# Optimization experiments

Measured on AMD Instinct MI355X. Metric: run time of the kernel, lower is better.

## Reference

```python
import jax, jax.numpy as jnp
import numpy as np

HEAD_NUM = 16

def setup_inputs() -> dict:
    key = jax.random.key(0)
    ks = jax.random.split(key, 5)
    B, N, D = 2, 2048, 1024
    x = jax.random.normal(ks[0], (B, N, D), dtype=jnp.float32)
    scale = 0.02
    W_q = jax.random.normal(ks[1], (D, D), dtype=jnp.float32) * scale
    W_k = jax.random.normal(ks[2], (D, D), dtype=jnp.float32) * scale
    W_v = jax.random.normal(ks[3], (D, D), dtype=jnp.float32) * scale
    W_o = jax.random.normal(ks[4], (D, D), dtype=jnp.float32) * scale
    return {"x": x, "W_q": W_q, "W_k": W_k, "W_v": W_v, "W_o": W_o}

def reference(x, W_q, W_k, W_v, W_o):
    B, N, D = x.shape
    H = HEAD_NUM
    hd = D // H  # head_dim
    inv_sqrt_hd = 1.0 / np.sqrt(hd).astype(np.float32)

    def split_head(t):
        # einops 'b n (d h) -> b h n d' : head index is the INNER factor
        return t.reshape(B, N, hd, H).transpose(0, 3, 1, 2)  # [B,H,N,hd]

    # nn.Linear(bias=False): y = x @ W.T
    Q = split_head(x @ W_q.T)
    K = split_head(x @ W_k.T)
    V = split_head(x @ W_v.T)

    scores = jnp.einsum('bhnd,bhmd->bhnm', Q, K) * inv_sqrt_hd  # [B,H,N,N]
    attn = jax.nn.softmax(scores, axis=-1)
    heads = jnp.einsum('bhnm,bhmd->bhnd', attn, V)  # [B,H,N,hd]

    # einops 'b h n d -> b n (h d)' : head index is the OUTER factor here
    concat = heads.transpose(0, 2, 1, 3).reshape(B, N, D)
    return concat @ W_o.T
```

## Files before the change

### kernel.cpp

```cpp
#include <hip/hip_runtime.h>
#include <hip/hip_bf16.h>

typedef __bf16 bf16_t;
typedef __attribute__((ext_vector_type(8))) __bf16 bf16x8;
typedef __attribute__((ext_vector_type(4))) __bf16 bf16x4;
typedef __attribute__((ext_vector_type(4))) float f32x4;
typedef __attribute__((ext_vector_type(16))) float f32x16;

#define MFMA16(A,B,C) __builtin_amdgcn_mfma_f32_16x16x32_bf16((A),(B),(C),0,0,0)
#define MFMA32(A,B,C) __builtin_amdgcn_mfma_f32_32x32x16_bf16((A),(B),(C),0,0,0)

#define BATCH 2
#define SEQ 2048
#define DMODEL 1024
#define NHEAD 16
#define HDIM 64
#define MROWS (BATCH * SEQ)

__device__ __forceinline__ void async16(const bf16_t* g, bf16_t* l) {
    __builtin_amdgcn_global_load_lds(
        (const __attribute__((address_space(1))) unsigned int*)g,
        (__attribute__((address_space(3))) unsigned int*)l, 16, 0, 0);
}

__device__ __forceinline__ bf16x8 ldsA32(const bf16_t* base, int row, int chunk) {
    return *(const bf16x8*)&base[row * 32 + ((chunk ^ ((row >> 1) & 3)) << 3)];
}
__device__ __forceinline__ bf16x8 ldsA64(const bf16_t* base, int row, int chunk) {
    return *(const bf16x8*)&base[row * 64 + ((chunk ^ (row & 7)) << 3)];
}

__device__ __forceinline__ unsigned pk(float a, float b) {
    union { unsigned u; bf16_t h[2]; } t;
    t.h[0] = (bf16_t)a;
    t.h[1] = (bf16_t)b;
    return t.u;
}

__global__ void split_kernel(const float* __restrict__ x, const float* __restrict__ Wq,
                             const float* __restrict__ Wk, const float* __restrict__ Wv,
                             const float* __restrict__ Wo, bf16_t* __restrict__ xh,
                             bf16_t* __restrict__ wh) {
    int blk = blockIdx.x;
    if (blk < 4096) {
        int i = blk * 256 + threadIdx.x;
        f32x4 v = ((const f32x4*)x)[i];
        bf16x4 h;
#pragma unroll
        for (int c = 0; c < 4; ++c) h[c] = (bf16_t)v[c];
        ((bf16x4*)xh)[i] = h;
        return;
    }
    int e = blk - 4096;
    int z = e >> 10;
    int i = (e & 1023) * 256 + threadIdx.x;
    const float* src = (z == 0) ? Wq : (z == 1) ? Wk : (z == 2) ? Wv : Wo;
    const float scale = (z == 0) ? 0.125f * 1.44269504088896f : 1.0f;
    int row = i >> 8, col4 = i & 255;
    int r_src;
    if (z < 3) {
        int h = row >> 6, d = row & 63;
        r_src = 16 * d + h;
    } else {
        r_src = row;
    }
    f32x4 v = ((const f32x4*)src)[r_src * 256 + col4];
    bf16x4 h4;
#pragma unroll
    for (int c = 0; c < 4; ++c) h4[c] = (bf16_t)(v[c] * scale);
    ((bf16x4*)(wh + (size_t)z * DMODEL * DMODEL))[i] = h4;
}

__global__ __launch_bounds__(256)
void gemm_qkv_kernel(const bf16_t* __restrict__ Ah, const bf16_t* __restrict__ Bh0,
                     bf16_t* __restrict__ Coh0, int M, int Nn, int Kk) {
    __shared__ __align__(16) bf16_t smem[2][8192];

    const int z = blockIdx.z;
    const bf16_t* Bh = Bh0 + (size_t)z * Nn * Kk;
    const int m0 = blockIdx.y * 128, n0 = blockIdx.x * 128;
    const int tid = threadIdx.x;
    const int wave = tid >> 6, lane = tid & 63, lq = lane >> 4, ln = lane & 15;
    const int wr = wave >> 1, wc = wave & 1;

    const bf16_t* g_ptr[4];
    int l_off[4];
#pragma unroll
    for (int q = 0; q < 4; ++q) {
        int e = wave * 4 + q;
        int a = e >> 3, u = e & 7;
        int C = u * 64 + lane;
        int r = C >> 2, p = C & 3;
        int c = p ^ ((r >> 1) & 3);
        g_ptr[q] = (a == 0 ? Ah + (size_t)(m0 + r) * Kk
                           : Bh + (size_t)(n0 + r) * Kk) + c * 8;
        l_off[q] = a * 4096 + u * 512;
    }

    f32x4 acc[4][4] = {};

#pragma unroll
    for (int q = 0; q < 4; ++q)
        async16(g_ptr[q], &smem[0][l_off[q]]);

    const int NIT = Kk / 32;
    for (int j = 0; j < NIT; ++j) {
        __syncthreads();
        if (j + 1 < NIT) {
#pragma unroll
            for (int q = 0; q < 4; ++q)
                async16(g_ptr[q] + (j + 1) * 32, &smem[(j + 1) & 1][l_off[q]]);
        }
        const bf16_t* cur = smem[j & 1];

        bf16x8 ah[4], bh[4];
#pragma unroll
        for (int t = 0; t < 4; ++t) {
            ah[t] = ldsA32(cur, wr * 64 + t * 16 + ln, lq);
            bh[t] = ldsA32(cur + 4096, wc * 64 + t * 16 + ln, lq);
        }
#pragma unroll
        for (int tm = 0; tm < 4; ++tm)
#pragma unroll
            for (int tn = 0; tn < 4; ++tn)
                acc[tm][tn] = MFMA16(ah[tm], bh[tn], acc[tm][tn]);
    }

#pragma unroll
    for (int tm = 0; tm < 4; ++tm)
#pragma unroll
        for (int tn = 0; tn < 4; ++tn)
#pragma unroll
            for (int p = 0; p < 4; ++p) {
                int gm = m0 + wr * 64 + tm * 16 + lq * 4 + p;
                int gn = n0 + wc * 64 + tn * 16 + ln;
                Coh0[(size_t)z * M * Nn + (size_t)gm * Nn + gn] =
                    (bf16_t)acc[tm][tn][p];
            }
}

__global__ __launch_bounds__(256)
void gemm_out_kernel(const bf16_t* __restrict__ Ah, const bf16_t* __restrict__ Bh,
                     float* __restrict__ Cf, int M, int Nn, int Kk) {
    __shared__ __align__(16) bf16_t smem[2][6144];

    const int m0 = blockIdx.y * 64, n0 = blockIdx.x * 128;
    const int tid = threadIdx.x;
    const int wave = tid >> 6, lane = tid & 63, lq = lane >> 4, ln = lane & 15;
    const int wr = wave >> 1, wc = wave & 1;

    const bf16_t* g_ptr[3];
    int l_off[3];
#pragma unroll
    for (int q = 0; q < 3; ++q) {
        int e = wave * 3 + q;
        const bf16_t* arr;
        int u, rowbase, lb;
        if (e < 4) { arr = Ah; u = e;     rowbase = m0; lb = 0; }
        else       { arr = Bh; u = e - 4; rowbase = n0; lb = 2048; }
        int r = u * 16 + (lane >> 2), p = lane & 3;
        int c = p ^ ((r >> 1) & 3);
        g_ptr[q] = arr + (size_t)(rowbase + r) * Kk + c * 8;
        l_off[q] = lb + u * 512;
    }

    f32x4 acc[2][4] = {};

#pragma unroll
    for (int q = 0; q < 3; ++q)
        async16(g_ptr[q], &smem[0][l_off[q]]);

    const int NIT = Kk / 32;
    for (int j = 0; j < NIT; ++j) {
        __syncthreads();
        if (j + 1 < NIT) {
#pragma unroll
            for (int q = 0; q < 3; ++q)
                async16(g_ptr[q] + (j + 1) * 32, &smem[(j + 1) & 1][l_off[q]]);
        }
        const bf16_t* cur = smem[j & 1];

        bf16x8 ah[2], bh[4];
#pragma unroll
        for (int t = 0; t < 2; ++t)
            ah[t] = ldsA32(cur, wr * 32 + t * 16 + ln, lq);
#pragma unroll
        for (int t = 0; t < 4; ++t)
            bh[t] = ldsA32(cur + 2048, wc * 64 + t * 16 + ln, lq);
#pragma unroll
        for (int tm = 0; tm < 2; ++tm)
#pragma unroll
            for (int tn = 0; tn < 4; ++tn)
                acc[tm][tn] = MFMA16(ah[tm], bh[tn], acc[tm][tn]);
    }

#pragma unroll
    for (int tm = 0; tm < 2; ++tm)
#pragma unroll
        for (int tn = 0; tn < 4; ++tn)
#pragma unroll
            for (int p = 0; p < 4; ++p) {
                int gm = m0 + wr * 32 + tm * 16 + lq * 4 + p;
                int gn = n0 + wc * 64 + tn * 16 + ln;
                Cf[(size_t)gm * Nn + gn] = acc[tm][tn][p];
            }
}

__global__ __launch_bounds__(256)
void vtrans_kernel(const bf16_t* __restrict__ Vn, bf16_t* __restrict__ Vt) {
    __shared__ bf16_t t[64][66];
    const int bh = blockIdx.y;
    const int b = bh >> 4, h = bh & 15;
    const int n0 = blockIdx.x * 64;
    const int tid = threadIdx.x;
#pragma unroll
    for (int it = 0; it < 2; ++it) {
        int c = it * 256 + tid;
        int r = c >> 3, p = c & 7;
        *(bf16x8*)&t[r][p * 8] =
            *(const bf16x8*)&Vn[((size_t)(b * SEQ + n0 + r)) * DMODEL + h * HDIM + p * 8];
    }
    __syncthreads();
#pragma unroll
    for (int it = 0; it < 2; ++it) {
        int c = it * 256 + tid;
        int d = c >> 3, p = c & 7;
        bf16x8 v;
#pragma unroll
        for (int e = 0; e < 8; ++e) v[e] = t[p * 8 + e][d];
        *(bf16x8*)&Vt[((size_t)(bh * HDIM + d)) * SEQ + n0 + p * 8] = v;
    }
}

__global__ __launch_bounds__(512, 4)
void attn_kernel(const bf16_t* __restrict__ Qh, const bf16_t* __restrict__ Kh,
                 const bf16_t* __restrict__ Vt, bf16_t* __restrict__ Ch) {
    __shared__ __align__(16) bf16_t smem[2][2][8192];

    const int bh = blockIdx.y;
    const int b = bh >> 4, h = bh & 15;
    const int q0 = blockIdx.x * 128;
    const int tid = threadIdx.x;
    const int g = tid >> 8;
    const int wv = (tid >> 6) & 3;
    const int lane = tid & 63;
    const int ln32 = lane & 31, hl = lane >> 5;

    bf16x8 qfh[4];
    {
        size_t qrow = ((size_t)(b * SEQ + q0 + wv * 32 + ln32)) * DMODEL +
                      h * HDIM + hl * 8;
#pragma unroll
        for (int c = 0; c < 4; ++c)
            qfh[c] = *(const bf16x8*)&Qh[qrow + c * 16];
    }
    bf16x8 ones;
#pragma unroll
    for (int e = 0; e < 8; ++e) ones[e] = (bf16_t)1.0f;

    bf16_t* gsm = &smem[g][0][0];
    const bf16_t* g_base[4];
    int l_off[4];
    size_t g_step[4];
#pragma unroll
    for (int q = 0; q < 4; ++q) {
        int e = wv * 4 + q;
        int a = e >> 3, u = e & 7;
        int r = u * 8 + (lane >> 3), p = lane & 7;
        int c = p ^ (r & 7);
        if (a == 0) {
            g_base[q] = Kh + ((size_t)(b * SEQ + g * 1024 + r)) * DMODEL +
                        h * HDIM + c * 8;
            l_off[q] = u * 512;
            g_step[q] = (size_t)64 * DMODEL;
        } else {
            g_base[q] = Vt + ((size_t)(bh * HDIM + r)) * SEQ + g * 1024 + c * 8;
            l_off[q] = 4096 + u * 512;
            g_step[q] = 64;
        }
    }

    f32x16 o[2], o_ones;
#pragma unroll
    for (int dt = 0; dt < 2; ++dt)
#pragma unroll
        for (int r = 0; r < 16; ++r) o[dt][r] = 0.0f;
#pragma unroll
    for (int r = 0; r < 16; ++r) o_ones[r] = 0.0f;

#pragma unroll
    for (int q = 0; q < 4; ++q)
        async16(g_base[q], gsm + l_off[q]);

    for (int j = 0; j < 16; ++j) {
        __syncthreads();
        if (j < 15) {
#pragma unroll
            for (int q = 0; q < 4; ++q)
                async16(g_base[q] + (j + 1) * g_step[q],
                        gsm + ((j + 1) & 1) * 8192 + l_off[q]);
        }
        const bf16_t* Kc = gsm + (j & 1) * 8192;
        const bf16_t* Vc = Kc + 4096;

        bf16x8 pfrag[4];
#pragma unroll
        for (int kt = 0; kt < 2; ++kt) {
            f32x16 st;
#pragma unroll
            for (int r = 0; r < 16; ++r) st[r] = 0.0f;
#pragma unroll
            for (int c = 0; c < 4; ++c) {
                bf16x8 kh = ldsA64(Kc, kt * 32 + ln32, 2 * c + hl);
                st = MFMA32(kh, qfh[c], st);
            }
            float pexp[16];
#pragma unroll
            for (int r = 0; r < 16; ++r)
                pexp[r] = __builtin_amdgcn_exp2f(st[r]);
#pragma unroll
            for (int s1 = 0; s1 < 2; ++s1) {
                unsigned lo01 = pk(pexp[8 * s1 + 0], pexp[8 * s1 + 1]);
                unsigned lo23 = pk(pexp[8 * s1 + 2], pexp[8 * s1 + 3]);
                unsigned hi01 = pk(pexp[8 * s1 + 4], pexp[8 * s1 + 5]);
                unsigned hi23 = pk(pexp[8 * s1 + 6], pexp[8 * s1 + 7]);
                unsigned sa = hl ? lo01 : hi01;
                unsigned sb = hl ? lo23 : hi23;
                unsigned ra = (unsigned)__shfl_xor((int)sa, 32);
                unsigned rb = (unsigned)__shfl_xor((int)sb, 32);
                union { bf16x8 v; unsigned u[4]; } outv;
                outv.u[0] = hl ? ra : lo01;
                outv.u[1] = hl ? rb : lo23;
                outv.u[2] = hl ? hi01 : ra;
                outv.u[3] = hl ? hi23 : rb;
                pfrag[kt * 2 + s1] = outv.v;
            }
        }
#pragma unroll
        for (int s = 0; s < 4; ++s) {
            bf16x8 va0 = ldsA64(Vc, ln32, 2 * s + hl);
            bf16x8 va1 = ldsA64(Vc, 32 + ln32, 2 * s + hl);
            o[0] = MFMA32(va0, pfrag[s], o[0]);
            o[1] = MFMA32(va1, pfrag[s], o[1]);
            o_ones = MFMA32(ones, pfrag[s], o_ones);
        }
    }

    float rs = o_ones[0];

    __syncthreads();
    float* cbuf = (float*)smem;
    float* rbuf = cbuf + 8192;
    if (g == 1) {
#pragma unroll
        for (int dt = 0; dt < 2; ++dt)
#pragma unroll
            for (int r = 0; r < 16; ++r) {
                int d = dt * 32 + (r & 3) + 8 * (r >> 2) + 4 * hl;
                cbuf[d * 128 + wv * 32 + ln32] = o[dt][r];
            }
        if (hl == 0) rbuf[wv * 32 + ln32] = rs;
    }
    __syncthreads();
    float inv = 0.0f;
    if (g == 0) {
#pragma unroll
        for (int dt = 0; dt < 2; ++dt)
#pragma unroll
            for (int r = 0; r < 16; ++r) {
                int d = dt * 32 + (r & 3) + 8 * (r >> 2) + 4 * hl;
                o[dt][r] += cbuf[d * 128 + wv * 32 + ln32];
            }
        inv = 1.0f / (rs + rbuf[wv * 32 + ln32]);
    }
    __syncthreads();
    float* fbuf = (float*)smem;
    if (g == 0) {
#pragma unroll
        for (int dh = 0; dh < 2; ++dh)
#pragma unroll
            for (int r = 0; r < 16; ++r) {
                int d_loc = (r & 3) + 8 * (r >> 2) + 4 * hl;
                fbuf[dh * 4224 + wv * 1056 + ln32 * 33 + d_loc] = o[dh][r] * inv;
            }
    }
    __syncthreads();
    {
        int gw = tid >> 6;
        int dh = gw >> 2, w = gw & 3;
#pragma unroll
        for (int qq = 0; qq < 16; ++qq) {
            int qrow = hl * 16 + qq;
            float v = fbuf[dh * 4224 + w * 1056 + qrow * 33 + ln32];
            size_t gidx = ((size_t)(b * SEQ + q0 + w * 32 + qrow)) * DMODEL +
                          h * HDIM + dh * 32 + ln32;
            Ch[gidx] = (bf16_t)v;
        }
    }
}

extern "C" void kernel_launch(void* const* d_in, const int* in_sizes, int n_in,
                              void* d_out, int out_size, void* d_ws, size_t ws_size,
                              hipStream_t stream) {
    const float* x  = (const float*)d_in[0];
    const float* Wq = (const float*)d_in[1];
    const float* Wk = (const float*)d_in[2];
    const float* Wv = (const float*)d_in[3];
    const float* Wo = (const float*)d_in[4];
    float* out = (float*)d_out;

    char* ws = (char*)d_ws;
    size_t off = 0;
    auto alloc = [&](size_t bytes) -> bf16_t* {
        bf16_t* p = (bf16_t*)(ws + off);
        off += (bytes + 255) & ~(size_t)255;
        return p;
    };
    const size_t XE = (size_t)MROWS * DMODEL;
    const size_t WE = (size_t)DMODEL * DMODEL;

    bf16_t* xh  = alloc(XE * 2);
    bf16_t* wh  = alloc(4 * WE * 2);
    bf16_t* qnh = alloc(3 * XE * 2);
    bf16_t* vth = alloc(XE * 2);
    bf16_t* ch  = alloc(XE * 2);
    (void)ws_size; (void)in_sizes; (void)n_in; (void)out_size;

    split_kernel<<<8192, 256, 0, stream>>>(x, Wq, Wk, Wv, Wo, xh, wh);

    gemm_qkv_kernel<<<dim3(DMODEL / 128, MROWS / 128, 3), 256, 0, stream>>>(
        xh, wh, qnh, MROWS, DMODEL, DMODEL);

    vtrans_kernel<<<dim3(SEQ / 64, BATCH * NHEAD), 256, 0, stream>>>(qnh + 2 * XE, vth);

    attn_kernel<<<dim3(SEQ / 128, BATCH * NHEAD), 512, 0, stream>>>(
        qnh, qnh + XE, vth, ch);

    gemm_out_kernel<<<dim3(DMODEL / 128, MROWS / 64), 256, 0, stream>>>(
        ch, wh + 3 * WE, out, MROWS, DMODEL, DMODEL);
}
```

Baseline: 184.7 us.

## Switch GEMMs to 32x32 MFMA and compute softmax row sums with VALU adds

Both the QKV and output projection GEMMs now use the 32x32x16 bf16 MFMA instead of 16x16x32 tiles. This cuts the LDS fragment loads per MFMA and uses the larger, more efficient matrix instruction. In attention, the extra MFMA that multiplied P by a ones vector to get row sums is replaced by accumulating exp values in a register plus a cross-half shuffle. This saves a third of the PV MFMAs at the cost of some VALU adds. The row sum now uses the fp32 exp values rather than the bf16-rounded ones, which changes numerics slightly.

```diff
diff --git a/kernel.cpp b/kernel.cpp
--- a/kernel.cpp
+++ b/kernel.cpp
@@ -7,7 +7,6 @@
 typedef __attribute__((ext_vector_type(4))) float f32x4;
 typedef __attribute__((ext_vector_type(16))) float f32x16;
 
-#define MFMA16(A,B,C) __builtin_amdgcn_mfma_f32_16x16x32_bf16((A),(B),(C),0,0,0)
 #define MFMA32(A,B,C) __builtin_amdgcn_mfma_f32_32x32x16_bf16((A),(B),(C),0,0,0)
 
 #define BATCH 2
@@ -80,7 +79,8 @@
     const bf16_t* Bh = Bh0 + (size_t)z * Nn * Kk;
     const int m0 = blockIdx.y * 128, n0 = blockIdx.x * 128;
     const int tid = threadIdx.x;
-    const int wave = tid >> 6, lane = tid & 63, lq = lane >> 4, ln = lane & 15;
+    const int wave = tid >> 6, lane = tid & 63;
+    const int ln32 = lane & 31, hl = lane >> 5;
     const int wr = wave >> 1, wc = wave & 1;
 
     const bf16_t* g_ptr[4];
@@ -97,7 +97,13 @@
         l_off[q] = a * 4096 + u * 512;
     }
 
-    f32x4 acc[4][4] = {};
+    f32x16 acc[2][2];
+#pragma unroll
+    for (int mt = 0; mt < 2; ++mt)
+#pragma unroll
+        for (int nt = 0; nt < 2; ++nt)
+#pragma unroll
+            for (int r = 0; r < 16; ++r) acc[mt][nt][r] = 0.0f;
 
 #pragma unroll
     for (int q = 0; q < 4; ++q)
@@ -113,29 +119,33 @@
         }
         const bf16_t* cur = smem[j & 1];
 
-        bf16x8 ah[4], bh[4];
-#pragma unroll
-        for (int t = 0; t < 4; ++t) {
-            ah[t] = ldsA32(cur, wr * 64 + t * 16 + ln, lq);
-            bh[t] = ldsA32(cur + 4096, wc * 64 + t * 16 + ln, lq);
-        }
-#pragma unroll
-        for (int tm = 0; tm < 4; ++tm)
-#pragma unroll
-            for (int tn = 0; tn < 4; ++tn)
-                acc[tm][tn] = MFMA16(ah[tm], bh[tn], acc[tm][tn]);
-    }
-
-#pragma unroll
-    for (int tm = 0; tm < 4; ++tm)
-#pragma unroll
-        for (int tn = 0; tn < 4; ++tn)
-#pragma unroll
-            for (int p = 0; p < 4; ++p) {
-                int gm = m0 + wr * 64 + tm * 16 + lq * 4 + p;
-                int gn = n0 + wc * 64 + tn * 16 + ln;
+        bf16x8 a[2][2], b[2][2];
+#pragma unroll
+        for (int t = 0; t < 2; ++t)
+#pragma unroll
+            for (int kc = 0; kc < 2; ++kc) {
+                a[t][kc] = ldsA32(cur, wr * 64 + t * 32 + ln32, kc * 2 + hl);
+                b[t][kc] = ldsA32(cur + 4096, wc * 64 + t * 32 + ln32, kc * 2 + hl);
+            }
+#pragma unroll
+        for (int mt = 0; mt < 2; ++mt)
+#pragma unroll
+            for (int nt = 0; nt < 2; ++nt)
+#pragma unroll
+                for (int kc = 0; kc < 2; ++kc)
+                    acc[mt][nt] = MFMA32(a[mt][kc], b[nt][kc], acc[mt][nt]);
+    }
+
+#pragma unroll
+    for (int mt = 0; mt < 2; ++mt)
+#pragma unroll
+        for (int nt = 0; nt < 2; ++nt)
+#pragma unroll
+            for (int r = 0; r < 16; ++r) {
+                int gm = m0 + wr * 64 + mt * 32 + (r & 3) + 8 * (r >> 2) + 4 * hl;
+                int gn = n0 + wc * 64 + nt * 32 + ln32;
                 Coh0[(size_t)z * M * Nn + (size_t)gm * Nn + gn] =
-                    (bf16_t)acc[tm][tn][p];
+                    (bf16_t)acc[mt][nt][r];
             }
 }
 
@@ -146,7 +156,8 @@
 
     const int m0 = blockIdx.y * 64, n0 = blockIdx.x * 128;
     const int tid = threadIdx.x;
-    const int wave = tid >> 6, lane = tid & 63, lq = lane >> 4, ln = lane & 15;
+    const int wave = tid >> 6, lane = tid & 63;
+    const int ln32 = lane & 31, hl = lane >> 5;
     const int wr = wave >> 1, wc = wave & 1;
 
     const bf16_t* g_ptr[3];
@@ -164,7 +175,11 @@
         l_off[q] = lb + u * 512;
     }
 
-    f32x4 acc[2][4] = {};
+    f32x16 acc[2];
+#pragma unroll
+    for (int nt = 0; nt < 2; ++nt)
+#pragma unroll
+        for (int r = 0; r < 16; ++r) acc[nt][r] = 0.0f;
 
 #pragma unroll
     for (int q = 0; q < 3; ++q)
@@ -180,30 +195,29 @@
         }
         const bf16_t* cur = smem[j & 1];
 
-        bf16x8 ah[2], bh[4];
-#pragma unroll
-        for (int t = 0; t < 2; ++t)
-            ah[t] = ldsA32(cur, wr * 32 + t * 16 + ln, lq);
-#pragma unroll
-        for (int t = 0; t < 4; ++t)
-            bh[t] = ldsA32(cur + 2048, wc * 64 + t * 16 + ln, lq);
-#pragma unroll
-        for (int tm = 0; tm < 2; ++tm)
-#pragma unroll
-            for (int tn = 0; tn < 4; ++tn)
-                acc[tm][tn] = MFMA16(ah[tm], bh[tn], acc[tm][tn]);
-    }
-
-#pragma unroll
-    for (int tm = 0; tm < 2; ++tm)
-#pragma unroll
-        for (int tn = 0; tn < 4; ++tn)
-#pragma unroll
-            for (int p = 0; p < 4; ++p) {
-                int gm = m0 + wr * 32 + tm * 16 + lq * 4 + p;
-                int gn = n0 + wc * 64 + tn * 16 + ln;
-                Cf[(size_t)gm * Nn + gn] = acc[tm][tn][p];
-            }
+        bf16x8 a[2], b[2][2];
+#pragma unroll
+        for (int kc = 0; kc < 2; ++kc) {
+            a[kc] = ldsA32(cur, wr * 32 + ln32, kc * 2 + hl);
+#pragma unroll
+            for (int nt = 0; nt < 2; ++nt)
+                b[nt][kc] = ldsA32(cur + 2048, wc * 64 + nt * 32 + ln32, kc * 2 + hl);
+        }
+#pragma unroll
+        for (int nt = 0; nt < 2; ++nt)
+#pragma unroll
+            for (int kc = 0; kc < 2; ++kc)
+                acc[nt] = MFMA32(a[kc], b[nt][kc], acc[nt]);
+    }
+
+#pragma unroll
+    for (int nt = 0; nt < 2; ++nt)
+#pragma unroll
+        for (int r = 0; r < 16; ++r) {
+            int gm = m0 + wr * 32 + (r & 3) + 8 * (r >> 2) + 4 * hl;
+            int gn = n0 + wc * 64 + nt * 32 + ln32;
+            Cf[(size_t)gm * Nn + gn] = acc[nt][r];
+        }
 }
 
 __global__ __launch_bounds__(256)
@@ -254,9 +268,6 @@
         for (int c = 0; c < 4; ++c)
             qfh[c] = *(const bf16x8*)&Qh[qrow + c * 16];
     }
-    bf16x8 ones;
-#pragma unroll
-    for (int e = 0; e < 8; ++e) ones[e] = (bf16_t)1.0f;
 
     bf16_t* gsm = &smem[g][0][0];
     const bf16_t* g_base[4];
@@ -280,13 +291,12 @@
         }
     }
 
-    f32x16 o[2], o_ones;
+    f32x16 o[2];
 #pragma unroll
     for (int dt = 0; dt < 2; ++dt)
 #pragma unroll
         for (int r = 0; r < 16; ++r) o[dt][r] = 0.0f;
-#pragma unroll
-    for (int r = 0; r < 16; ++r) o_ones[r] = 0.0f;
+    float rs = 0.0f;
 
 #pragma unroll
     for (int q = 0; q < 4; ++q)
@@ -316,8 +326,10 @@
             }
             float pexp[16];
 #pragma unroll
-            for (int r = 0; r < 16; ++r)
+            for (int r = 0; r < 16; ++r) {
                 pexp[r] = __builtin_amdgcn_exp2f(st[r]);
+                rs += pexp[r];
+            }
 #pragma unroll
             for (int s1 = 0; s1 < 2; ++s1) {
                 unsigned lo01 = pk(pexp[8 * s1 + 0], pexp[8 * s1 + 1]);
@@ -342,11 +354,10 @@
             bf16x8 va1 = ldsA64(Vc, 32 + ln32, 2 * s + hl);
             o[0] = MFMA32(va0, pfrag[s], o[0]);
             o[1] = MFMA32(va1, pfrag[s], o[1]);
-            o_ones = MFMA32(ones, pfrag[s], o_ones);
-        }
-    }
-
-    float rs = o_ones[0];
+        }
+    }
+
+    rs += __shfl_xor(rs, 32);
 
     __syncthreads();
     float* cbuf = (float*)smem;
```

After: 187.2 us. About the same (+1.3%).
